# Performance work log

Measured on AMD Instinct MI355X. Metric: run time of the kernel, lower is better.

## Reference

```python
import jax, jax.numpy as jnp
import numpy as np

N_FFT = 512
HOP = 128
WIN_LENGTH = 512  # == n_fft, so no window padding needed


def hann_periodic(n):
    # torch.hann_window default is periodic=True
    return (0.5 - 0.5 * jnp.cos(2.0 * jnp.pi * jnp.arange(n) / n)).astype(jnp.float32)


def setup_inputs() -> dict:
    key = jax.random.key(0)
    k1, _ = jax.random.split(key)
    B, C, F, T = 16, 2, N_FFT // 2 + 1, 2048
    X = jax.random.normal(k1, (B, C, F, T, 2), dtype=jnp.float32)
    window = hann_periodic(WIN_LENGTH)
    return {"X": X, "window": window}


def istft(X, window):
    # X: (B, C, F, T, 2) real+imag; onesided, center=True, normalized=False
    Xc = jax.lax.complex(X[..., 0], X[..., 1])          # (B, C, F, T)
    frames = jnp.fft.irfft(Xc, n=N_FFT, axis=-2)        # (B, C, n_fft, T)
    frames = frames * window[None, None, :, None]       # windowed frames
    frames = jnp.moveaxis(frames, -2, -1)               # (B, C, T, n_fft)

    T = frames.shape[-2]
    full_len = N_FFT + (T - 1) * HOP
    # overlap-add scatter indices: (T, n_fft)
    idx = (jnp.arange(T) * HOP)[:, None] + jnp.arange(N_FFT)[None, :]

    y = jnp.zeros(frames.shape[:2] + (full_len,), frames.dtype).at[..., idx].add(frames)
    # window-envelope normalization (sum of squared windows, overlap-added)
    env = jnp.zeros((full_len,), window.dtype).at[idx].add(
        jnp.broadcast_to(window * window, (T, N_FFT)))

    pad = N_FFT // 2  # center=True trims n_fft//2 from both ends
    return y[..., pad:full_len - pad] / env[pad:full_len - pad]


def reference(X, window):
    return istft(X, window)  # (B, C, (T-1)*hop)
```

## Files before the change

### kernel.cpp

```cpp
#include <hip/hip_runtime.h>
#include <hip/hip_bf16.h>

#define NFFT    512
#define HOPSZ   128
#define FBINS   257
#define TFR     2048
#define NBC     32
#define OUTLEN  262016
#define SPAD    256

typedef __bf16 bf16x8 __attribute__((ext_vector_type(8)));
typedef float  f32x4  __attribute__((ext_vector_type(4)));

static __device__ __forceinline__ float bf2f(unsigned short u) {
    union { unsigned int i; float f; } x; x.i = (unsigned int)u << 16; return x.f;
}

__device__ __forceinline__ void gld_lds16(const void* g, void* l) {
    __builtin_amdgcn_global_load_lds(
        (const __attribute__((address_space(1))) unsigned int*)g,
        (__attribute__((address_space(3))) unsigned int*)l, 16, 0, 0);
}

__global__ __launch_bounds__(256) void k_wgen(const float* __restrict__ wnd,
                                              uint4* __restrict__ Wf) {
    const int gid  = blockIdx.x * 256 + threadIdx.x;
    const int lane = gid & 63;
    const int rt   = (gid >> 6) & 31;
    const int ks   = gid >> 11;
    const int n    = rt * 16 + (lane & 15);
    const int kb   = ks * 32 + ((lane >> 4) << 2);
    const float wn = wnd[n] * (1.0f / 512.0f);
    union { uint4 u; unsigned short h[8]; } o;
    #pragma unroll
    for (int j = 0; j < 8; ++j) {
        const int k = kb + (j & 3) + 16 * (j >> 2);
        float val = 0.0f;
        if (k < 2 * FBINS) {
            const int f = k >> 1;
            const bool edge = (f == 0) || (f == 256);
            const float cf = edge ? 1.0f : 2.0f;
            const int m = (f * n) & (NFFT - 1);
            const float ang = (float)m * 0.01227184630308513f;
            float s, c;
            __sincosf(ang, &s, &c);
            val = (k & 1) ? (edge ? 0.0f : -cf * wn * s) : (cf * wn * c);
        }
        __hip_bfloat16 hb = __float2bfloat16(val);
        o.h[j] = *(unsigned short*)&hb;
    }
    Wf[gid] = o.u;
}

__global__ __launch_bounds__(512, 4) void k_mm(
    const float* __restrict__ X,
    const uint4* __restrict__ Wf,
    __hip_bfloat16* __restrict__ frames)
{
    __shared__ uint4 Ab[2][32][64];
    __shared__ uint4 Bb[2][4][64];

    const int tid  = threadIdx.x;
    const int lane = tid & 63;
    const int w    = tid >> 6;
    const int q    = lane >> 4;
    const int rlo  = lane & 15;

    const int bid = blockIdx.x;
    const int id  = (bid & 7) * 128 + (bid >> 3);
    const int bc  = id >> 5;
    const int t0b = (id & 31) << 6;

    const float2* __restrict__ X2 = (const float2*)X + (size_t)bc * FBINS * TFR;

    const int sf  = tid >> 4;
    const int st  = tid & 15;
    const int r2  = (2 * sf) & 31;
    const int skk = sf >> 4;
    const int sq  = (r2 & 15) >> 2;
    const int sj  = ((r2 & 2) >> 1) + (((r2 >> 4) & 1) << 1);
    unsigned int* __restrict__ BbU = (unsigned int*)Bb;

    f32x4 acc[4][4] = {};

    for (int ks = 0; ks < 8; ++ks) {
        __syncthreads();
        float2 xv[4];
        const float2* xb = X2 + (size_t)(ks * 32 + sf) * TFR + t0b + st;
        #pragma unroll
        for (int d = 0; d < 4; ++d) xv[d] = xb[16 * d];
        #pragma unroll
        for (int s = 0; s < 2; ++s) {
            const uint4* src = Wf + (size_t)(2 * ks + s) * 2048;
            uint4* dst = &Ab[s][0][0];
            #pragma unroll
            for (int r = 0; r < 4; ++r)
                gld_lds16(src + r * 512 + tid, dst + r * 512 + tid);
        }
        #pragma unroll
        for (int d = 0; d < 4; ++d) {
            union { unsigned int u; __hip_bfloat16 h[2]; } p;
            p.h[0] = __float2bfloat16(xv[d].x);
            p.h[1] = __float2bfloat16(xv[d].y);
            BbU[(((((skk << 2) + sq) << 6) + st + (d << 4)) << 2) + sj] = p.u;
        }
        __syncthreads();
        #pragma unroll
        for (int kk = 0; kk < 2; ++kk) {
            uint4 a[4], b[4];
            #pragma unroll
            for (int ni = 0; ni < 4; ++ni) b[ni] = Bb[kk][q][ni * 16 + rlo];
            #pragma unroll
            for (int mi = 0; mi < 4; ++mi) a[mi] = Ab[kk][4 * w + mi][lane];
            #pragma unroll
            for (int mi = 0; mi < 4; ++mi)
                #pragma unroll
                for (int ni = 0; ni < 4; ++ni)
                    acc[mi][ni] = __builtin_amdgcn_mfma_f32_16x16x32_bf16(
                        __builtin_bit_cast(bf16x8, a[mi]),
                        __builtin_bit_cast(bf16x8, b[ni]), acc[mi][ni], 0, 0, 0);
        }
    }

    unsigned short* fb = (unsigned short*)frames;
    #pragma unroll
    for (int mi = 0; mi < 4; ++mi) {
        const int nbase = (w << 6) + (mi << 4) + (q << 2);
        #pragma unroll
        for (int ni = 0; ni < 4; ++ni) {
            const int t = t0b + ni * 16 + rlo;
            union { ushort4 u; __hip_bfloat16 hh[4]; } pk;
            pk.hh[0] = __float2bfloat16(acc[mi][ni][0]);
            pk.hh[1] = __float2bfloat16(acc[mi][ni][1]);
            pk.hh[2] = __float2bfloat16(acc[mi][ni][2]);
            pk.hh[3] = __float2bfloat16(acc[mi][ni][3]);
            *(ushort4*)(fb + (((size_t)(bc * TFR + t)) << 9) + nbase) = pk.u;
        }
    }
}

__global__ __launch_bounds__(256) void k_ola(
    const __hip_bfloat16* __restrict__ frames,
    const float* __restrict__ wnd,
    const float* __restrict__ X,
    float* __restrict__ out)
{
    const int bc = blockIdx.y;
    const int o  = (blockIdx.x * 256 + threadIdx.x) * 4;
    if (o >= OUTLEN) return;
    const int s   = o + SPAD;
    const int tb_ = s >> 7;
    const int nb  = s & (HOPSZ - 1);
    const unsigned short* fb = (const unsigned short*)frames + (size_t)bc * TFR * NFFT;
    const float* Xre = X + (((size_t)bc * FBINS + 256) * TFR) * 2;
    const float sA = ((nb & 1) ? -1.0f : 1.0f) * (1.0f / 512.0f);
    float y0 = 0.f, y1 = 0.f, y2 = 0.f, y3 = 0.f;
    float e0 = 0.f, e1 = 0.f, e2 = 0.f, e3 = 0.f;
    #pragma unroll
    for (int r = 0; r < 4; ++r) {
        const int t = tb_ - r;
        if ((unsigned)t > (unsigned)(TFR - 1)) continue;
        const int n = nb + (r << 7);
        ushort4 v = *(const ushort4*)(fb + (size_t)t * NFFT + n);
        float4  wv = *(const float4*)(wnd + n);
        const float c = sA * Xre[2 * t];
        y0 += bf2f(v.x) + c * wv.x; e0 += wv.x * wv.x;
        y1 += bf2f(v.y) - c * wv.y; e1 += wv.y * wv.y;
        y2 += bf2f(v.z) + c * wv.z; e2 += wv.z * wv.z;
        y3 += bf2f(v.w) - c * wv.w; e3 += wv.w * wv.w;
    }
    float4 res = make_float4(y0 / e0, y1 / e1, y2 / e2, y3 / e3);
    *(float4*)(out + (size_t)bc * OUTLEN + o) = res;
}

extern "C" void kernel_launch(void* const* d_in, const int* in_sizes, int n_in,
                              void* d_out, int out_size, void* d_ws, size_t ws_size,
                              hipStream_t stream) {
    (void)in_sizes; (void)n_in; (void)out_size; (void)ws_size;
    const float* X   = (const float*)d_in[0];
    const float* wnd = (const float*)d_in[1];
    float* out = (float*)d_out;

    uint4* Wf = (uint4*)d_ws;
    __hip_bfloat16* frames = (__hip_bfloat16*)((char*)d_ws + (1 << 20));

    k_wgen<<<136, 256, 0, stream>>>(wnd, Wf);
    k_mm<<<1024, 512, 0, stream>>>(X, Wf, frames);
    k_ola<<<dim3((OUTLEN / 4 + 255) / 256, NBC), 256, 0, stream>>>(frames, wnd, X, out);
}
```

Before: 84.22 us.

## Double-buffer GEMM K-loop to overlap loads with MFMA compute

Restructures the k_mm main loop from 8 steps of two K-slices with two barriers each into 16 single-slice steps using ping-pong LDS buffers. The next slice's Wf (direct global-to-LDS) and X loads are issued before computing the current slice, and X is packed into the alternate buffer afterwards, leaving one barrier per step. The aim is to hide global memory latency behind MFMA work. It also changes the X load pattern to 32 contiguous t per row and reorganizes the B tile layout. In exchange it uses more registers for the prefetched values and has a fully unrolled loop.

Result: no change. 85.81 us (+1.9%).

```diff
diff --git a/kernel.cpp b/kernel.cpp
--- a/kernel.cpp
+++ b/kernel.cpp
@@ -58,7 +58,7 @@
     __hip_bfloat16* __restrict__ frames)
 {
     __shared__ uint4 Ab[2][32][64];
-    __shared__ uint4 Bb[2][4][64];
+    __shared__ uint4 Bb[2][4][4][16];
 
     const int tid  = threadIdx.x;
     const int lane = tid & 63;
@@ -73,52 +73,68 @@
 
     const float2* __restrict__ X2 = (const float2*)X + (size_t)bc * FBINS * TFR;
 
-    const int sf  = tid >> 4;
-    const int st  = tid & 15;
-    const int r2  = (2 * sf) & 31;
-    const int skk = sf >> 4;
-    const int sq  = (r2 & 15) >> 2;
-    const int sj  = ((r2 & 2) >> 1) + (((r2 >> 4) & 1) << 1);
+    const int sf  = tid >> 5;
+    const int stt = tid & 31;
+    const int sq  = ((2 * sf) & 15) >> 2;
+    const int sjw = (sf & 1) + 2 * (sf >> 3);
     unsigned int* __restrict__ BbU = (unsigned int*)Bb;
 
-    f32x4 acc[4][4] = {};
-
-    for (int ks = 0; ks < 8; ++ks) {
-        __syncthreads();
-        float2 xv[4];
-        const float2* xb = X2 + (size_t)(ks * 32 + sf) * TFR + t0b + st;
-        #pragma unroll
-        for (int d = 0; d < 4; ++d) xv[d] = xb[16 * d];
-        #pragma unroll
-        for (int s = 0; s < 2; ++s) {
-            const uint4* src = Wf + (size_t)(2 * ks + s) * 2048;
-            uint4* dst = &Ab[s][0][0];
-            #pragma unroll
-            for (int r = 0; r < 4; ++r)
-                gld_lds16(src + r * 512 + tid, dst + r * 512 + tid);
-        }
-        #pragma unroll
-        for (int d = 0; d < 4; ++d) {
+    f32x4  acc[4][4] = {};
+    float2 xvA[2], xvB[2];
+
+    auto issueA = [&](int ks, int buf) {
+        const uint4* src = Wf + (size_t)ks * 2048;
+        uint4* dst = &Ab[buf][0][0];
+        #pragma unroll
+        for (int r = 0; r < 4; ++r)
+            gld_lds16(src + r * 512 + tid, dst + r * 512 + tid);
+    };
+    auto issueB = [&](int ks, float2* xv) {
+        const float2* xb = X2 + (size_t)(ks * 16 + sf) * TFR + t0b + stt;
+        xv[0] = xb[0];
+        xv[1] = xb[32];
+    };
+    auto packB = [&](int buf, float2* xv) {
+        #pragma unroll
+        for (int d = 0; d < 2; ++d) {
             union { unsigned int u; __hip_bfloat16 h[2]; } p;
             p.h[0] = __float2bfloat16(xv[d].x);
             p.h[1] = __float2bfloat16(xv[d].y);
-            BbU[(((((skk << 2) + sq) << 6) + st + (d << 4)) << 2) + sj] = p.u;
-        }
-        __syncthreads();
-        #pragma unroll
-        for (int kk = 0; kk < 2; ++kk) {
-            uint4 a[4], b[4];
+            const int tile = (stt >> 4) + 2 * d;
+            BbU[((((buf * 4 + sq) * 4 + tile) * 16) + (stt & 15)) * 4 + sjw] = p.u;
+        }
+    };
+    auto compute = [&](int buf) {
+        uint4 a[4], b[4];
+        #pragma unroll
+        for (int ni = 0; ni < 4; ++ni) b[ni] = Bb[buf][q][ni][rlo];
+        #pragma unroll
+        for (int mi = 0; mi < 4; ++mi) a[mi] = Ab[buf][4 * w + mi][lane];
+        #pragma unroll
+        for (int mi = 0; mi < 4; ++mi)
             #pragma unroll
-            for (int ni = 0; ni < 4; ++ni) b[ni] = Bb[kk][q][ni * 16 + rlo];
-            #pragma unroll
-            for (int mi = 0; mi < 4; ++mi) a[mi] = Ab[kk][4 * w + mi][lane];
-            #pragma unroll
-            for (int mi = 0; mi < 4; ++mi)
-                #pragma unroll
-                for (int ni = 0; ni < 4; ++ni)
-                    acc[mi][ni] = __builtin_amdgcn_mfma_f32_16x16x32_bf16(
-                        __builtin_bit_cast(bf16x8, a[mi]),
-                        __builtin_bit_cast(bf16x8, b[ni]), acc[mi][ni], 0, 0, 0);
+            for (int ni = 0; ni < 4; ++ni)
+                acc[mi][ni] = __builtin_amdgcn_mfma_f32_16x16x32_bf16(
+                    __builtin_bit_cast(bf16x8, a[mi]),
+                    __builtin_bit_cast(bf16x8, b[ni]), acc[mi][ni], 0, 0, 0);
+    };
+
+    issueB(0, xvA);
+    issueA(0, 0);
+    packB(0, xvA);
+    __syncthreads();
+
+    #pragma unroll
+    for (int ks = 0; ks < 16; ++ks) {
+        const int cur = ks & 1;
+        if (ks < 15) {
+            if (ks & 1) issueB(ks + 1, xvA); else issueB(ks + 1, xvB);
+            issueA(ks + 1, cur ^ 1);
+        }
+        compute(cur);
+        if (ks < 15) {
+            if (ks & 1) packB(cur ^ 1, xvA); else packB(cur ^ 1, xvB);
+            __syncthreads();
         }
     }
 
```

## Split GEMM tile across two blocks and stage X via direct LDS loads

Applied to the files above, without the earlier changes.

The frame GEMM now uses 256-thread blocks, each computing half of the 512 output rows, with twice as many blocks and half-sized K steps. The fp32 X tile is loaded straight into LDS with global_load_lds and converted to bf16 at fragment-build time, so the register round trip and scattered LDS stores are gone. The cost is that each X tile is now read by two blocks, the K loop runs more iterations with more barriers, and the bf16 conversion is repeated per wave.

Result: faster. 81.65 us (-3.0%).

```diff
diff --git a/kernel.cpp b/kernel.cpp
--- a/kernel.cpp
+++ b/kernel.cpp
@@ -52,13 +52,13 @@
     Wf[gid] = o.u;
 }
 
-__global__ __launch_bounds__(512, 4) void k_mm(
+__global__ __launch_bounds__(256, 4) void k_mm(
     const float* __restrict__ X,
     const uint4* __restrict__ Wf,
     __hip_bfloat16* __restrict__ frames)
 {
-    __shared__ uint4 Ab[2][32][64];
-    __shared__ uint4 Bb[2][4][64];
+    __shared__ uint4  Ab[1024];
+    __shared__ float2 Bf[16][64];
 
     const int tid  = threadIdx.x;
     const int lane = tid & 63;
@@ -67,65 +67,66 @@
     const int rlo  = lane & 15;
 
     const int bid = blockIdx.x;
-    const int id  = (bid & 7) * 128 + (bid >> 3);
-    const int bc  = id >> 5;
-    const int t0b = (id & 31) << 6;
+    const int id  = (bid & 7) * 256 + (bid >> 3);
+    const int m     = id & 1;
+    const int panel = (id >> 1) & 31;
+    const int bc    = id >> 6;
+    const int t0b   = panel << 6;
 
     const float2* __restrict__ X2 = (const float2*)X + (size_t)bc * FBINS * TFR;
 
-    const int sf  = tid >> 4;
-    const int st  = tid & 15;
-    const int r2  = (2 * sf) & 31;
-    const int skk = sf >> 4;
-    const int sq  = (r2 & 15) >> 2;
-    const int sj  = ((r2 & 2) >> 1) + (((r2 >> 4) & 1) << 1);
-    unsigned int* __restrict__ BbU = (unsigned int*)Bb;
+    const int br = tid >> 5;
+    const int bck = tid & 31;
 
     f32x4 acc[4][4] = {};
 
-    for (int ks = 0; ks < 8; ++ks) {
+    for (int ks = 0; ks < 16; ++ks) {
         __syncthreads();
-        float2 xv[4];
-        const float2* xb = X2 + (size_t)(ks * 32 + sf) * TFR + t0b + st;
+        const uint4* asrc = Wf + (size_t)ks * 2048 + m * 1024;
         #pragma unroll
-        for (int d = 0; d < 4; ++d) xv[d] = xb[16 * d];
+        for (int r = 0; r < 4; ++r)
+            gld_lds16(asrc + r * 256 + tid, &Ab[r * 256 + tid]);
+        {
+            const float2* b0 = X2 + (size_t)(ks * 16 + br) * TFR + t0b + 2 * bck;
+            gld_lds16(b0,                    &Bf[br][2 * bck]);
+            gld_lds16(b0 + (size_t)8 * TFR,  &Bf[br + 8][2 * bck]);
+        }
+        __syncthreads();
+        uint4 a[4], b[4];
         #pragma unroll
-        for (int s = 0; s < 2; ++s) {
-            const uint4* src = Wf + (size_t)(2 * ks + s) * 2048;
-            uint4* dst = &Ab[s][0][0];
-            #pragma unroll
-            for (int r = 0; r < 4; ++r)
-                gld_lds16(src + r * 512 + tid, dst + r * 512 + tid);
+        for (int ni = 0; ni < 4; ++ni) {
+            const float2* Bp = &Bf[2 * q][ni * 16 + rlo];
+            float2 v0 = Bp[0];
+            float2 v1 = Bp[64];
+            float2 v2 = Bp[8 * 64];
+            float2 v3 = Bp[9 * 64];
+            union { unsigned short h[8]; uint4 u; } pk;
+            __hip_bfloat16 t;
+            t = __float2bfloat16(v0.x); pk.h[0] = *(unsigned short*)&t;
+            t = __float2bfloat16(v0.y); pk.h[1] = *(unsigned short*)&t;
+            t = __float2bfloat16(v1.x); pk.h[2] = *(unsigned short*)&t;
+            t = __float2bfloat16(v1.y); pk.h[3] = *(unsigned short*)&t;
+            t = __float2bfloat16(v2.x); pk.h[4] = *(unsigned short*)&t;
+            t = __float2bfloat16(v2.y); pk.h[5] = *(unsigned short*)&t;
+            t = __float2bfloat16(v3.x); pk.h[6] = *(unsigned short*)&t;
+            t = __float2bfloat16(v3.y); pk.h[7] = *(unsigned short*)&t;
+            b[ni] = pk.u;
         }
         #pragma unroll
-        for (int d = 0; d < 4; ++d) {
-            union { unsigned int u; __hip_bfloat16 h[2]; } p;
-            p.h[0] = __float2bfloat16(xv[d].x);
-            p.h[1] = __float2bfloat16(xv[d].y);
-            BbU[(((((skk << 2) + sq) << 6) + st + (d << 4)) << 2) + sj] = p.u;
-        }
-        __syncthreads();
+        for (int mi = 0; mi < 4; ++mi) a[mi] = Ab[(4 * w + mi) * 64 + lane];
         #pragma unroll
-        for (int kk = 0; kk < 2; ++kk) {
-            uint4 a[4], b[4];
+        for (int mi = 0; mi < 4; ++mi)
             #pragma unroll
-            for (int ni = 0; ni < 4; ++ni) b[ni] = Bb[kk][q][ni * 16 + rlo];
-            #pragma unroll
-            for (int mi = 0; mi < 4; ++mi) a[mi] = Ab[kk][4 * w + mi][lane];
-            #pragma unroll
-            for (int mi = 0; mi < 4; ++mi)
-                #pragma unroll
-                for (int ni = 0; ni < 4; ++ni)
-                    acc[mi][ni] = __builtin_amdgcn_mfma_f32_16x16x32_bf16(
-                        __builtin_bit_cast(bf16x8, a[mi]),
-                        __builtin_bit_cast(bf16x8, b[ni]), acc[mi][ni], 0, 0, 0);
-        }
+            for (int ni = 0; ni < 4; ++ni)
+                acc[mi][ni] = __builtin_amdgcn_mfma_f32_16x16x32_bf16(
+                    __builtin_bit_cast(bf16x8, a[mi]),
+                    __builtin_bit_cast(bf16x8, b[ni]), acc[mi][ni], 0, 0, 0);
     }
 
     unsigned short* fb = (unsigned short*)frames;
     #pragma unroll
     for (int mi = 0; mi < 4; ++mi) {
-        const int nbase = (w << 6) + (mi << 4) + (q << 2);
+        const int nbase = m * 256 + (w << 6) + (mi << 4) + (q << 2);
         #pragma unroll
         for (int ni = 0; ni < 4; ++ni) {
             const int t = t0b + ni * 16 + rlo;
@@ -185,6 +186,6 @@
     __hip_bfloat16* frames = (__hip_bfloat16*)((char*)d_ws + (1 << 20));
 
     k_wgen<<<136, 256, 0, stream>>>(wnd, Wf);
-    k_mm<<<1024, 512, 0, stream>>>(X, Wf, frames);
+    k_mm<<<2048, 256, 0, stream>>>(X, Wf, frames);
     k_ola<<<dim3((OUTLEN / 4 + 255) / 256, NBC), 256, 0, stream>>>(frames, wnd, X, out);
 }
```

## Fuse inverse-DFT matmul with overlap-add using overlapping frame panels in LDS

Applied to the files above, without the earlier changes.

Merges the MFMA frame-synthesis kernel and the overlap-add kernel into one. Each block computes 64 frames with a stride of 61, so that three frames overlap with the neighbouring panel. The windowed frames stay in LDS and the block writes only the output samples it fully owns. This removes the bf16 frames round trip through global memory (about 64 MB) and one kernel launch. In exchange it recomputes about 5% of the frames, grows LDS to 72 KB per block (which can cut occupancy), and uses scalar, non-vectorised output stores.

New measurement: 79.39 us. -5.7%, faster.

```diff
diff --git a/kernel.cpp b/kernel.cpp
--- a/kernel.cpp
+++ b/kernel.cpp
@@ -8,6 +8,9 @@
 #define NBC     32
 #define OUTLEN  262016
 #define SPAD    256
+#define NPANEL  34
+#define PSTR    61
+#define FROW    532
 
 typedef __bf16 bf16x8 __attribute__((ext_vector_type(8)));
 typedef float  f32x4  __attribute__((ext_vector_type(4)));
@@ -52,13 +55,18 @@
     Wf[gid] = o.u;
 }
 
-__global__ __launch_bounds__(512, 4) void k_mm(
+__global__ __launch_bounds__(512, 4) void k_fused(
     const float* __restrict__ X,
     const uint4* __restrict__ Wf,
-    __hip_bfloat16* __restrict__ frames)
+    const float* __restrict__ wnd,
+    float* __restrict__ out)
 {
-    __shared__ uint4 Ab[2][32][64];
-    __shared__ uint4 Bb[2][4][64];
+    __shared__ __align__(16) char smem[73728];
+    uint4* Ab  = (uint4*)smem;
+    uint4* Bb4 = (uint4*)(smem + 65536);
+    unsigned int* BbU = (unsigned int*)(smem + 65536);
+    float* XreL = (float*)(smem + 68096);
+    float* wL   = (float*)(smem + 68352);
 
     const int tid  = threadIdx.x;
     const int lane = tid & 63;
@@ -67,9 +75,10 @@
     const int rlo  = lane & 15;
 
     const int bid = blockIdx.x;
-    const int id  = (bid & 7) * 128 + (bid >> 3);
-    const int bc  = id >> 5;
-    const int t0b = (id & 31) << 6;
+    const int id  = (bid & 7) * 136 + (bid >> 3);
+    const int panel = id % NPANEL;
+    const int bc    = id / NPANEL;
+    const int tp    = panel * PSTR;
 
     const float2* __restrict__ X2 = (const float2*)X + (size_t)bc * FBINS * TFR;
 
@@ -79,20 +88,22 @@
     const int skk = sf >> 4;
     const int sq  = (r2 & 15) >> 2;
     const int sj  = ((r2 & 2) >> 1) + (((r2 >> 4) & 1) << 1);
-    unsigned int* __restrict__ BbU = (unsigned int*)Bb;
 
     f32x4 acc[4][4] = {};
 
     for (int ks = 0; ks < 8; ++ks) {
         __syncthreads();
         float2 xv[4];
-        const float2* xb = X2 + (size_t)(ks * 32 + sf) * TFR + t0b + st;
         #pragma unroll
-        for (int d = 0; d < 4; ++d) xv[d] = xb[16 * d];
+        for (int d = 0; d < 4; ++d) {
+            int t = tp + st + (d << 4);
+            t = (t < TFR) ? t : (TFR - 1);
+            xv[d] = X2[(size_t)(ks * 32 + sf) * TFR + t];
+        }
         #pragma unroll
         for (int s = 0; s < 2; ++s) {
             const uint4* src = Wf + (size_t)(2 * ks + s) * 2048;
-            uint4* dst = &Ab[s][0][0];
+            uint4* dst = Ab + s * 2048;
             #pragma unroll
             for (int r = 0; r < 4; ++r)
                 gld_lds16(src + r * 512 + tid, dst + r * 512 + tid);
@@ -109,9 +120,9 @@
         for (int kk = 0; kk < 2; ++kk) {
             uint4 a[4], b[4];
             #pragma unroll
-            for (int ni = 0; ni < 4; ++ni) b[ni] = Bb[kk][q][ni * 16 + rlo];
+            for (int ni = 0; ni < 4; ++ni) b[ni] = Bb4[(kk * 4 + q) * 64 + ni * 16 + rlo];
             #pragma unroll
-            for (int mi = 0; mi < 4; ++mi) a[mi] = Ab[kk][4 * w + mi][lane];
+            for (int mi = 0; mi < 4; ++mi) a[mi] = Ab[(kk * 32 + 4 * w + mi) * 64 + lane];
             #pragma unroll
             for (int mi = 0; mi < 4; ++mi)
                 #pragma unroll
@@ -122,55 +133,51 @@
         }
     }
 
-    unsigned short* fb = (unsigned short*)frames;
+    __syncthreads();
     #pragma unroll
     for (int mi = 0; mi < 4; ++mi) {
-        const int nbase = (w << 6) + (mi << 4) + (q << 2);
+        const int n = (w << 6) + (mi << 4) + (q << 2);
         #pragma unroll
         for (int ni = 0; ni < 4; ++ni) {
-            const int t = t0b + ni * 16 + rlo;
+            const int lt = ni * 16 + rlo;
             union { ushort4 u; __hip_bfloat16 hh[4]; } pk;
             pk.hh[0] = __float2bfloat16(acc[mi][ni][0]);
             pk.hh[1] = __float2bfloat16(acc[mi][ni][1]);
             pk.hh[2] = __float2bfloat16(acc[mi][ni][2]);
             pk.hh[3] = __float2bfloat16(acc[mi][ni][3]);
-            *(ushort4*)(fb + (((size_t)(bc * TFR + t)) << 9) + nbase) = pk.u;
+            *(ushort4*)((unsigned short*)(smem + lt * (FROW * 2)) + n) = pk.u;
         }
     }
-}
+    if (tid < 64) {
+        int t = tp + tid;
+        t = (t < TFR) ? t : (TFR - 1);
+        XreL[tid] = X2[(size_t)256 * TFR + t].x;
+    }
+    wL[tid] = wnd[tid];
+    __syncthreads();
 
-__global__ __launch_bounds__(256) void k_ola(
-    const __hip_bfloat16* __restrict__ frames,
-    const float* __restrict__ wnd,
-    const float* __restrict__ X,
-    float* __restrict__ out)
-{
-    const int bc = blockIdx.y;
-    const int o  = (blockIdx.x * 256 + threadIdx.x) * 4;
-    if (o >= OUTLEN) return;
-    const int s   = o + SPAD;
-    const int tb_ = s >> 7;
-    const int nb  = s & (HOPSZ - 1);
-    const unsigned short* fb = (const unsigned short*)frames + (size_t)bc * TFR * NFFT;
-    const float* Xre = X + (((size_t)bc * FBINS + 256) * TFR) * 2;
-    const float sA = ((nb & 1) ? -1.0f : 1.0f) * (1.0f / 512.0f);
-    float y0 = 0.f, y1 = 0.f, y2 = 0.f, y3 = 0.f;
-    float e0 = 0.f, e1 = 0.f, e2 = 0.f, e3 = 0.f;
-    #pragma unroll
-    for (int r = 0; r < 4; ++r) {
-        const int t = tb_ - r;
-        if ((unsigned)t > (unsigned)(TFR - 1)) continue;
-        const int n = nb + (r << 7);
-        ushort4 v = *(const ushort4*)(fb + (size_t)t * NFFT + n);
-        float4  wv = *(const float4*)(wnd + n);
-        const float c = sA * Xre[2 * t];
-        y0 += bf2f(v.x) + c * wv.x; e0 += wv.x * wv.x;
-        y1 += bf2f(v.y) - c * wv.y; e1 += wv.y * wv.y;
-        y2 += bf2f(v.z) + c * wv.z; e2 += wv.z * wv.z;
-        y3 += bf2f(v.w) - c * wv.w; e3 += wv.w * wv.w;
+    const int olo = (panel == 0) ? 0 : tp * 128 + 128;
+    const int ohi = (panel == NPANEL - 1) ? OUTLEN : tp * 128 + 7936;
+    float* outb = out + (size_t)bc * OUTLEN;
+    for (int o = olo + tid; o < ohi; o += 512) {
+        const int s  = o + SPAD;
+        const int tb = s >> 7;
+        const int nb = s & (HOPSZ - 1);
+        const float sg = (s & 1) ? (-1.0f / 512.0f) : (1.0f / 512.0f);
+        float y = 0.f, e = 0.f;
+        #pragma unroll
+        for (int r = 0; r < 4; ++r) {
+            const int t  = tb - r;
+            const int lt = t - tp;
+            if ((unsigned)lt >= 64u || (unsigned)t >= (unsigned)TFR) continue;
+            const int n = nb + (r << 7);
+            const float wv = wL[n];
+            const float fv = bf2f(*((const unsigned short*)(smem + lt * (FROW * 2)) + n));
+            y += fv + sg * XreL[lt] * wv;
+            e += wv * wv;
+        }
+        outb[o] = y / e;
     }
-    float4 res = make_float4(y0 / e0, y1 / e1, y2 / e2, y3 / e3);
-    *(float4*)(out + (size_t)bc * OUTLEN + o) = res;
 }
 
 extern "C" void kernel_launch(void* const* d_in, const int* in_sizes, int n_in,
@@ -182,9 +189,7 @@
     float* out = (float*)d_out;
 
     uint4* Wf = (uint4*)d_ws;
-    __hip_bfloat16* frames = (__hip_bfloat16*)((char*)d_ws + (1 << 20));
 
     k_wgen<<<136, 256, 0, stream>>>(wnd, Wf);
-    k_mm<<<1024, 512, 0, stream>>>(X, Wf, frames);
-    k_ola<<<dim3((OUTLEN / 4 + 255) / 256, NBC), 256, 0, stream>>>(frames, wnd, X, out);
+    k_fused<<<NBC * NPANEL, 512, 0, stream>>>(X, Wf, wnd, out);
 }
```
